# Kernel optimization log

Hardware: AMD Instinct MI355X
Metric: run time of the kernel (lower is better)

The kernel has to match this reference:

```python
import jax, jax.numpy as jnp
import numpy as np


def _bce_with_logits(x, t):
    # numerically-stable binary_cross_entropy_with_logits, reduction='none'
    return jnp.maximum(x, 0.0) - x * t + jnp.log1p(jnp.exp(-jnp.abs(x)))


def _compute_weights(targets):
    """Replicates the scipy.ndimage.label / sum_labels weighting.

    4-connected component labeling (scipy default structure) via iterative
    min-label propagation, then per-pixel component area, then
    1 / (sqrt(area) + 1) with zeros replaced by the global mean of the
    nonzero sqrt-areas.
    """
    B, H, W = targets.shape
    HW = H * W  # sentinel label for background
    fg = targets > 0
    base = jnp.arange(HW, dtype=jnp.int32).reshape(1, H, W)
    lab0 = jnp.where(fg, base, HW).astype(jnp.int32)

    def cond(state):
        return state[1]

    def body(state):
        lab, _ = state
        p = jnp.pad(lab, ((0, 0), (1, 1), (1, 1)), constant_values=HW)
        nb = jnp.minimum(jnp.minimum(p[:, :-2, 1:-1], p[:, 2:, 1:-1]),
                         jnp.minimum(p[:, 1:-1, :-2], p[:, 1:-1, 2:]))
        new = jnp.where(fg, jnp.minimum(lab, nb), HW)
        return new, jnp.any(new != lab)

    lab, _ = jax.lax.while_loop(cond, body, (lab0, jnp.array(True)))

    def per_sample_area(lab_i, fg_i):
        sizes = jax.ops.segment_sum(fg_i.ravel().astype(jnp.float32),
                                    lab_i.ravel(), num_segments=HW + 1)
        return sizes[lab_i]  # [H, W] area of each pixel's component

    area = jax.vmap(per_sample_area)(lab, fg)
    area = jnp.where(fg, area, 0.0)

    w = jnp.sqrt(area)
    nz = w > 0
    # global (whole-tensor) mean of nonzero sqrt-areas, as in the torch code
    mean_nz = jnp.sum(jnp.where(nz, w, 0.0)) / jnp.maximum(
        jnp.sum(nz.astype(jnp.float32)), 1.0)
    w_filled = jnp.where(nz, w, mean_nz)
    return 1.0 / (w_filled + 1.0)


def setup_inputs() -> dict:
    key = jax.random.key(0)
    k1, k2 = jax.random.split(key)
    B, H, W = 32, 512, 512
    inputs = jax.random.normal(k1, (B, H, W), dtype=jnp.float32)
    # sparse binary mask (subcritical density -> small blobs, like vessels)
    targets = (jax.random.uniform(k2, (B, H, W)) < 0.3).astype(jnp.float32)
    return {"inputs": inputs, "targets": targets}


def reference(inputs, targets):
    weights = _compute_weights(targets)
    bce = _bce_with_logits(inputs, targets)
    return jnp.mean(weights * bce)
```

## Files before the change

kernel.cpp:

```cpp
#include <hip/hip_runtime.h>
#include <math.h>

static constexpr int IMG_W  = 512;
static constexpr int IMG_PX = 512 * 512;
static constexpr int NIMG   = 32;
static constexpr int TILE_W = 64;
static constexpr int TILE_H = 32;
static constexpr int TPX    = IMG_W / TILE_W;
static constexpr int TPY    = IMG_W / TILE_H;
static constexpr int TILES_PER_IMG = TPX * TPY;
static constexpr int FUSED_BLOCKS  = NIMG * TILES_PER_IMG;
static constexpr int ECAP_T  = 48;
static constexpr int SCAP    = 128;
static constexpr int NE      = TILES_PER_IMG * ECAP_T;
static constexpr int FLAGBIT = 1 << 30;
static constexpr int CNTMASK = FLAGBIT - 1;
static constexpr int TPIX    = TILE_W * TILE_H;


__device__ __forceinline__ int find_root_l(volatile int* sl, int x) {
    int p = sl[x];
    while (p != x) { x = p; p = sl[x]; }
    return p;
}

__device__ __forceinline__ void merge_l(int* sl, int a, int b) {
    while (true) {
        a = find_root_l(sl, a);
        b = find_root_l(sl, b);
        if (a == b) return;
        if (a < b) { int t = a; a = b; b = t; }
        int old = atomicMin(&sl[a], b);
        if (old == a) return;
        a = old;
    }
}

__device__ __forceinline__ void block_reduce_write(float s_fg, float s_bg,
                                                   float s_sq, float s_n,
                                                   double4* __restrict__ part,
                                                   int slot) {
    for (int o = 32; o > 0; o >>= 1) {
        s_fg += __shfl_down(s_fg, o, 64);
        s_bg += __shfl_down(s_bg, o, 64);
        s_sq += __shfl_down(s_sq, o, 64);
        s_n  += __shfl_down(s_n,  o, 64);
    }
    __shared__ double4 wsum[4];
    int wave = threadIdx.x >> 6;
    if ((threadIdx.x & 63) == 0)
        wsum[wave] = make_double4((double)s_fg, (double)s_bg, (double)s_sq, (double)s_n);
    __syncthreads();
    if (threadIdx.x == 0) {
        double4 b = wsum[0];
        for (int wv = 1; wv < 4; wv++) {
            b.x += wsum[wv].x; b.y += wsum[wv].y;
            b.z += wsum[wv].z; b.w += wsum[wv].w;
        }
        part[slot] = b;
    }
}

__device__ __forceinline__ float bce0_fast(float xx) {
    return fmaxf(xx, 0.f) + __logf(1.f + __expf(-fabsf(xx)));
}


__global__ __launch_bounds__(256) void ccl_fused(const float* __restrict__ t,
                                                 const float* __restrict__ x,
                                                 int* __restrict__ L,
                                                 int2* __restrict__ ilist,
                                                 int* __restrict__ blockcount,
                                                 int2* __restrict__ seams,
                                                 int* __restrict__ seamcount,
                                                 double4* __restrict__ part,
                                                 int* __restrict__ done) {
    __shared__ int   sl[TPIX];
    __shared__ int   cnt[TPIX];
    __shared__ float fsum[TPIX];
    __shared__ unsigned long long rowmask[TILE_H];
    __shared__ int   lcount, scount;

    int blk = blockIdx.x;
    int b   = blk / TILES_PER_IMG;
    int tid = blk % TILES_PER_IMG;
    int tY  = tid / TPX, tX = tid % TPX;
    int k   = threadIdx.x;
    int col = k & 63, wv = k >> 6;
    int base = b * IMG_PX + (tY * TILE_H) * IMG_W + tX * TILE_W;

    if (k == 0) { lcount = 0; scount = 0; }
    if (blk == 0 && k == 0) *done = 0;

    float xr[8];
    unsigned int fgbits = 0;
#pragma unroll
    for (int s = 0; s < 8; s++) {
        int row = wv * 8 + s;
        int jj  = row * TILE_W + col;
        int g   = base + row * IMG_W + col;
        float tv = t[g];
        xr[s] = x[g];
        bool fg = (tv != 0.f);
        fgbits |= (unsigned)fg << s;
        unsigned long long mask = __ballot(fg);
        if (col == 0) rowmask[row] = mask;
        int lab = jj;
        if (fg) {
            unsigned long long startm = mask & ~(mask << 1);
            unsigned long long low = (col == 63) ? ~0ULL : ((1ULL << (col + 1)) - 1ULL);
            lab = row * TILE_W + (63 - __clzll(startm & low));
        }
        sl[jj]   = lab;
        cnt[jj]  = 0;
        fsum[jj] = 0.f;
    }
    __syncthreads();

#pragma unroll
    for (int s = 0; s < 8; s++) {
        int row = wv * 8 + s;
        if (row == 0) continue;
        unsigned long long both = rowmask[row] & rowmask[row - 1];
        unsigned long long pairstart = both & ~(both << 1);
        if ((pairstart >> col) & 1ULL)
            merge_l(sl, row * TILE_W + col, (row - 1) * TILE_W + col);
    }
    __syncthreads();

#pragma unroll
    for (int s = 0; s < 8; s++) {
        int row = wv * 8 + s;
        unsigned long long mask = rowmask[row];
        unsigned long long startm = mask & ~(mask << 1);
        if ((startm >> col) & 1ULL) {
            unsigned long long inv = ~(mask >> col);
            int len = inv ? (__ffsll((long long)inv) - 1) : (64 - col);
            int jj = row * TILE_W + col;
            int r = find_root_l(sl, jj);
            sl[jj] = r;
            atomicAdd(&cnt[r], len);
        }
    }
    __syncthreads();

    {
        int r = -1, c = 0, dg = 0; bool owner = false;
        if      (k < 64)  { r = 0;          c = k;        dg = (tY > 0)       ? -IMG_W : 0; }
        else if (k < 128) { r = TILE_H - 1; c = k - 64;   dg = (tY < TPY - 1) ?  IMG_W : 0; owner = true; }
        else if (k < 160) { r = k - 128;    c = 0;        dg = (tX > 0)       ? -1     : 0; }
        else if (k < 192) { r = k - 160;    c = TILE_W-1; dg = (tX < TPX - 1) ?  1     : 0; owner = true; }
        if (r >= 0) {
            int g = base + r * IMG_W + c;
            bool fg = (rowmask[r] >> c) & 1ULL;
            if (fg) {
                int jj = r * TILE_W + c;
                int root = sl[sl[jj]];
                L[g] = base + (root >> 6) * IMG_W + (root & 63);
                if (dg != 0 && t[g + dg] != 0.f) {
                    atomicOr(&cnt[root], FLAGBIT);
                    if (owner) {
                        int s = atomicAdd(&scount, 1);
                        if (s < SCAP) seams[blk * SCAP + s] = make_int2(g, g + dg);
                    }
                }
            }
        }
    }
    __syncthreads();

    float s_fg = 0.f, s_bg = 0.f, s_sq = 0.f, s_n = 0.f;
#pragma unroll
    for (int s = 0; s < 8; s++) {
        int row = wv * 8 + s;
        int jj  = row * TILE_W + col;
        float xx = xr[s];
        float b0 = bce0_fast(xx);
        int s0   = sl[jj];
        int root = sl[s0];
        int cc   = cnt[root];
        bool fg  = (fgbits >> s) & 1u;
        float bce1 = b0 - xx;
        if (cc & FLAGBIT) {
            atomicAdd(&fsum[root], bce1);
        } else {
            float w   = sqrtf((float)cc);
            float inv = 1.f / (w + 1.f);
            s_fg += fg ? bce1 * inv : 0.f;
            s_bg += fg ? 0.f : b0;
            s_sq += w;
            s_n  += fg ? 1.f : 0.f;
        }
    }
    __syncthreads();

#pragma unroll
    for (int s = 0; s < 8; s++) {
        int jj = (wv * 8 + s) * TILE_W + col;
        if (sl[jj] == jj && (cnt[jj] & FLAGBIT)) {
            int slot = atomicAdd(&lcount, 1);
            if (slot < ECAP_T) {
                ilist[blk * ECAP_T + slot] =
                    make_int2(__float_as_int(fsum[jj]), cnt[jj] & CNTMASK);
                int g = base + (jj >> 6) * IMG_W + (jj & 63);
                L[g] = -(tid * ECAP_T + slot) - 2;
            }
        }
    }
    block_reduce_write(s_fg, s_bg, s_sq, s_n, part, blk);
    if (k == 0) { blockcount[blk] = min(lcount, ECAP_T); seamcount[blk] = min(scount, SCAP); }
}

__global__ __launch_bounds__(1024) void tail(const int* __restrict__ L,
                                             const int2* __restrict__ ilist,
                                             const int* __restrict__ blockcount,
                                             const int2* __restrict__ seams,
                                             const int* __restrict__ seamcount,
                                             const double4* __restrict__ part,
                                             double4* __restrict__ imgpart,
                                             int* __restrict__ done,
                                             float* __restrict__ out,
                                             int N) {
    __shared__ int parent[NE];
    __shared__ int areaL[NE];
    __shared__ int scEx[TILES_PER_IMG + 1];
    __shared__ int bcEx[TILES_PER_IMG + 1];
    int b = blockIdx.x, k = threadIdx.x;
    int tbase = b * TILES_PER_IMG;

    for (int i = k; i < NE; i += 1024) { parent[i] = i; areaL[i] = 0; }
    if (k < TILES_PER_IMG) {
        scEx[k + 1] = seamcount[tbase + k];
        bcEx[k + 1] = blockcount[tbase + k];
    }
    if (k == 0) { scEx[0] = 0; bcEx[0] = 0; }
    __syncthreads();
    for (int off = 1; off < TILES_PER_IMG; off <<= 1) {
        int vs = 0, vb = 0;
        if (k < TILES_PER_IMG && (int)k >= off) {
            vs = scEx[k + 1 - off];
            vb = bcEx[k + 1 - off];
        }
        __syncthreads();
        if (k < TILES_PER_IMG && (int)k >= off) {
            scEx[k + 1] += vs;
            bcEx[k + 1] += vb;
        }
        __syncthreads();
    }
    int nS = scEx[TILES_PER_IMG];
    int nE = bcEx[TILES_PER_IMG];

    for (int i = k; i < nS; i += 1024) {
        int lo = 0, hi = TILES_PER_IMG;
        while (hi - lo > 1) { int mid = (lo + hi) >> 1; if (i >= scEx[mid]) lo = mid; else hi = mid; }
        int slot = i - scEx[lo];
        int2 p = seams[(tbase + lo) * SCAP + slot];
        int v1 = L[p.x]; if (v1 >= 0) v1 = L[v1];
        int v2 = L[p.y]; if (v2 >= 0) v2 = L[v2];
        int e1 = -v1 - 2, e2 = -v2 - 2;
        if (e1 >= 0 && e1 < NE && e2 >= 0 && e2 < NE)
            merge_l(parent, e1, e2);
    }
    __syncthreads();

    for (int i = k; i < nE; i += 1024) {
        int lo = 0, hi = TILES_PER_IMG;
        while (hi - lo > 1) { int mid = (lo + hi) >> 1; if (i >= bcEx[mid]) lo = mid; else hi = mid; }
        int slot = i - bcEx[lo];
        int idx = lo * ECAP_T + slot;
        int2 ent = ilist[(tbase + lo) * ECAP_T + slot];
        atomicAdd(&areaL[find_root_l(parent, idx)], ent.y);
    }
    __syncthreads();

    float s_fg = 0.f, s_sq = 0.f, s_n = 0.f;
    for (int i = k; i < nE; i += 1024) {
        int lo = 0, hi = TILES_PER_IMG;
        while (hi - lo > 1) { int mid = (lo + hi) >> 1; if (i >= bcEx[mid]) lo = mid; else hi = mid; }
        int slot = i - bcEx[lo];
        int idx = lo * ECAP_T + slot;
        int2 ent = ilist[(tbase + lo) * ECAP_T + slot];
        float w = sqrtf((float)areaL[find_root_l(parent, idx)]);
        float c = (float)ent.y;
        s_fg += __int_as_float(ent.x) / (w + 1.f);
        s_sq += c * w;
        s_n  += c;
    }

    double fg = (double)s_fg, bg = 0.0, sq = (double)s_sq, nn = (double)s_n;
    if (k < TILES_PER_IMG) {
        double4 p = part[tbase + k];
        fg += p.x; bg += p.y; sq += p.z; nn += p.w;
    }
    for (int o = 32; o > 0; o >>= 1) {
        fg += __shfl_down(fg, o, 64);
        bg += __shfl_down(bg, o, 64);
        sq += __shfl_down(sq, o, 64);
        nn += __shfl_down(nn, o, 64);
    }
    __shared__ double4 f2[16];
    int wave = k >> 6;
    if ((k & 63) == 0) f2[wave] = make_double4(fg, bg, sq, nn);
    __syncthreads();
    if (k == 0) {
        double4 bb = f2[0];
        for (int wv = 1; wv < 16; wv++) {
            bb.x += f2[wv].x; bb.y += f2[wv].y;
            bb.z += f2[wv].z; bb.w += f2[wv].w;
        }
        imgpart[b] = bb;
    }

    __shared__ int amlast;
    __syncthreads();
    __threadfence();
    if (k == 0) amlast = (atomicAdd(done, 1) == NIMG - 1);
    __syncthreads();
    if (!amlast) return;
    __threadfence();
    double tfg = 0.0, tbg = 0.0, tsq = 0.0, tnn = 0.0;
    if (k < NIMG) {
        double4 p = imgpart[k];
        tfg = p.x; tbg = p.y; tsq = p.z; tnn = p.w;
    }
    if (k < 64) {
        for (int o = 32; o > 0; o >>= 1) {
            tfg += __shfl_down(tfg, o, 64);
            tbg += __shfl_down(tbg, o, 64);
            tsq += __shfl_down(tsq, o, 64);
            tnn += __shfl_down(tnn, o, 64);
        }
        if (k == 0) {
            double mean_nz = tsq / fmax(tnn, 1.0);
            double loss = (tfg + tbg / (mean_nz + 1.0)) / (double)N;
            out[0] = (float)loss;
        }
    }
}


extern "C" void kernel_launch(void* const* d_in, const int* in_sizes, int n_in,
                              void* d_out, int out_size, void* d_ws, size_t ws_size,
                              hipStream_t stream) {
    const float* x = (const float*)d_in[0];
    const float* t = (const float*)d_in[1];
    float* out = (float*)d_out;
    int N = in_sizes[0];

    int* L          = (int*)d_ws;
    double4* part   = (double4*)(L + N);
    double4* imgpart = part + FUSED_BLOCKS;
    int* blockcount = (int*)(imgpart + NIMG);
    int* seamcount  = blockcount + FUSED_BLOCKS;
    int* done       = seamcount + FUSED_BLOCKS;
    int2* ilist     = (int2*)(done + 4);
    int2* seams     = ilist + FUSED_BLOCKS * ECAP_T;

    ccl_fused<<<FUSED_BLOCKS, 256, 0, stream>>>(t, x, L, ilist, blockcount,
                                                seams, seamcount, part, done);
    tail<<<NIMG, 1024, 0, stream>>>(L, ilist, blockcount, seams, seamcount,
                                    part, imgpart, done, out, N);
}
```

Measured before the change: 154.8 us.

## Fuse per-image tail into CCL kernel via last-tile-block election

```diff
diff --git a/kernel.cpp b/kernel.cpp
--- a/kernel.cpp
+++ b/kernel.cpp
@@ -38,6 +38,7 @@
 
 __device__ __forceinline__ void block_reduce_write(float s_fg, float s_bg,
                                                    float s_sq, float s_n,
+                                                   double4* wsum,
                                                    double4* __restrict__ part,
                                                    int slot) {
     for (int o = 32; o > 0; o >>= 1) {
@@ -46,7 +47,6 @@
         s_sq += __shfl_down(s_sq, o, 64);
         s_n  += __shfl_down(s_n,  o, 64);
     }
-    __shared__ double4 wsum[4];
     int wave = threadIdx.x >> 6;
     if ((threadIdx.x & 63) == 0)
         wsum[wave] = make_double4((double)s_fg, (double)s_bg, (double)s_sq, (double)s_n);
@@ -74,12 +74,24 @@
                                                  int2* __restrict__ seams,
                                                  int* __restrict__ seamcount,
                                                  double4* __restrict__ part,
-                                                 int* __restrict__ done) {
-    __shared__ int   sl[TPIX];
-    __shared__ int   cnt[TPIX];
-    __shared__ float fsum[TPIX];
+                                                 double4* __restrict__ imgpart,
+                                                 int* __restrict__ done,
+                                                 float* __restrict__ out,
+                                                 int N) {
+    union SU {
+        struct { int sl[TPIX]; int cnt[TPIX]; float fsum[TPIX]; } c;
+        int parent[NE];
+    };
+    __shared__ SU su;
     __shared__ unsigned long long rowmask[TILE_H];
-    __shared__ int   lcount, scount;
+    __shared__ int   lcount, scount, elect;
+    __shared__ double4 wsum[4];
+    __shared__ int scEx[TILES_PER_IMG + 1];
+    __shared__ int bcEx[TILES_PER_IMG + 1];
+
+    int* sl    = su.c.sl;
+    int* cnt   = su.c.cnt;
+    float* fsum = su.c.fsum;
 
     int blk = blockIdx.x;
     int b   = blk / TILES_PER_IMG;
@@ -90,7 +102,6 @@
     int base = b * IMG_PX + (tY * TILE_H) * IMG_W + tX * TILE_W;
 
     if (k == 0) { lcount = 0; scount = 0; }
-    if (blk == 0 && k == 0) *done = 0;
 
     float xr[8];
     unsigned int fgbits = 0;
@@ -207,28 +218,20 @@
             }
         }
     }
-    block_reduce_write(s_fg, s_bg, s_sq, s_n, part, blk);
+    block_reduce_write(s_fg, s_bg, s_sq, s_n, wsum, part, blk);
     if (k == 0) { blockcount[blk] = min(lcount, ECAP_T); seamcount[blk] = min(scount, SCAP); }
-}
-
-__global__ __launch_bounds__(1024) void tail(const int* __restrict__ L,
-                                             const int2* __restrict__ ilist,
-                                             const int* __restrict__ blockcount,
-                                             const int2* __restrict__ seams,
-                                             const int* __restrict__ seamcount,
-                                             const double4* __restrict__ part,
-                                             double4* __restrict__ imgpart,
-                                             int* __restrict__ done,
-                                             float* __restrict__ out,
-                                             int N) {
-    __shared__ int parent[NE];
-    __shared__ int areaL[NE];
-    __shared__ int scEx[TILES_PER_IMG + 1];
-    __shared__ int bcEx[TILES_PER_IMG + 1];
-    int b = blockIdx.x, k = threadIdx.x;
+
+    __syncthreads();
+    __threadfence();
+    if (k == 0) elect = (atomicAdd(&done[b], 1) == TILES_PER_IMG - 1);
+    __syncthreads();
+    if (!elect) return;
+    __threadfence();
+
+    int* parent = su.parent;
     int tbase = b * TILES_PER_IMG;
 
-    for (int i = k; i < NE; i += 1024) { parent[i] = i; areaL[i] = 0; }
+    for (int i = k; i < NE; i += 256) parent[i] = i;
     if (k < TILES_PER_IMG) {
         scEx[k + 1] = seamcount[tbase + k];
         bcEx[k + 1] = blockcount[tbase + k];
@@ -237,12 +240,12 @@
     __syncthreads();
     for (int off = 1; off < TILES_PER_IMG; off <<= 1) {
         int vs = 0, vb = 0;
-        if (k < TILES_PER_IMG && (int)k >= off) {
+        if (k < TILES_PER_IMG && k >= off) {
             vs = scEx[k + 1 - off];
             vb = bcEx[k + 1 - off];
         }
         __syncthreads();
-        if (k < TILES_PER_IMG && (int)k >= off) {
+        if (k < TILES_PER_IMG && k >= off) {
             scEx[k + 1] += vs;
             bcEx[k + 1] += vb;
         }
@@ -251,11 +254,11 @@
     int nS = scEx[TILES_PER_IMG];
     int nE = bcEx[TILES_PER_IMG];
 
-    for (int i = k; i < nS; i += 1024) {
+    for (int i = k; i < nS; i += 256) {
         int lo = 0, hi = TILES_PER_IMG;
         while (hi - lo > 1) { int mid = (lo + hi) >> 1; if (i >= scEx[mid]) lo = mid; else hi = mid; }
         int slot = i - scEx[lo];
-        int2 p = seams[(tbase + lo) * SCAP + slot];
+        int2 p = seams[(size_t)(tbase + lo) * SCAP + slot];
         int v1 = L[p.x]; if (v1 >= 0) v1 = L[v1];
         int v2 = L[p.y]; if (v2 >= 0) v2 = L[v2];
         int e1 = -v1 - 2, e2 = -v2 - 2;
@@ -264,31 +267,35 @@
     }
     __syncthreads();
 
-    for (int i = k; i < nE; i += 1024) {
+    int* areaG = (int*)(seams + (size_t)tbase * SCAP);
+    for (int i = k; i < NE; i += 256) areaG[i] = 0;
+    __syncthreads();
+
+    for (int i = k; i < nE; i += 256) {
         int lo = 0, hi = TILES_PER_IMG;
         while (hi - lo > 1) { int mid = (lo + hi) >> 1; if (i >= bcEx[mid]) lo = mid; else hi = mid; }
         int slot = i - bcEx[lo];
         int idx = lo * ECAP_T + slot;
-        int2 ent = ilist[(tbase + lo) * ECAP_T + slot];
-        atomicAdd(&areaL[find_root_l(parent, idx)], ent.y);
-    }
-    __syncthreads();
-
-    float s_fg = 0.f, s_sq = 0.f, s_n = 0.f;
-    for (int i = k; i < nE; i += 1024) {
+        int2 ent = ilist[(size_t)(tbase + lo) * ECAP_T + slot];
+        atomicAdd(&areaG[find_root_l(parent, idx)], ent.y);
+    }
+    __syncthreads();
+
+    float t_fg = 0.f, t_sq = 0.f, t_n = 0.f;
+    for (int i = k; i < nE; i += 256) {
         int lo = 0, hi = TILES_PER_IMG;
         while (hi - lo > 1) { int mid = (lo + hi) >> 1; if (i >= bcEx[mid]) lo = mid; else hi = mid; }
         int slot = i - bcEx[lo];
         int idx = lo * ECAP_T + slot;
-        int2 ent = ilist[(tbase + lo) * ECAP_T + slot];
-        float w = sqrtf((float)areaL[find_root_l(parent, idx)]);
+        int2 ent = ilist[(size_t)(tbase + lo) * ECAP_T + slot];
+        float w = sqrtf((float)areaG[find_root_l(parent, idx)]);
         float c = (float)ent.y;
-        s_fg += __int_as_float(ent.x) / (w + 1.f);
-        s_sq += c * w;
-        s_n  += c;
-    }
-
-    double fg = (double)s_fg, bg = 0.0, sq = (double)s_sq, nn = (double)s_n;
+        t_fg += __int_as_float(ent.x) / (w + 1.f);
+        t_sq += c * w;
+        t_n  += c;
+    }
+
+    double fg = (double)t_fg, bg = 0.0, sq = (double)t_sq, nn = (double)t_n;
     if (k < TILES_PER_IMG) {
         double4 p = part[tbase + k];
         fg += p.x; bg += p.y; sq += p.z; nn += p.w;
@@ -299,26 +306,25 @@
         sq += __shfl_down(sq, o, 64);
         nn += __shfl_down(nn, o, 64);
     }
-    __shared__ double4 f2[16];
     int wave = k >> 6;
-    if ((k & 63) == 0) f2[wave] = make_double4(fg, bg, sq, nn);
+    if ((k & 63) == 0) wsum[wave] = make_double4(fg, bg, sq, nn);
     __syncthreads();
     if (k == 0) {
-        double4 bb = f2[0];
-        for (int wv = 1; wv < 16; wv++) {
-            bb.x += f2[wv].x; bb.y += f2[wv].y;
-            bb.z += f2[wv].z; bb.w += f2[wv].w;
+        double4 bb = wsum[0];
+        for (int wv2 = 1; wv2 < 4; wv2++) {
+            bb.x += wsum[wv2].x; bb.y += wsum[wv2].y;
+            bb.z += wsum[wv2].z; bb.w += wsum[wv2].w;
         }
         imgpart[b] = bb;
     }
 
-    __shared__ int amlast;
     __syncthreads();
     __threadfence();
-    if (k == 0) amlast = (atomicAdd(done, 1) == NIMG - 1);
-    __syncthreads();
-    if (!amlast) return;
+    if (k == 0) elect = (atomicAdd(&done[NIMG], 1) == NIMG - 1);
+    __syncthreads();
+    if (!elect) return;
     __threadfence();
+
     double tfg = 0.0, tbg = 0.0, tsq = 0.0, tnn = 0.0;
     if (k < NIMG) {
         double4 p = imgpart[k];
@@ -354,11 +360,12 @@
     int* blockcount = (int*)(imgpart + NIMG);
     int* seamcount  = blockcount + FUSED_BLOCKS;
     int* done       = seamcount + FUSED_BLOCKS;
-    int2* ilist     = (int2*)(done + 4);
+    int2* ilist     = (int2*)(done + 64);
     int2* seams     = ilist + FUSED_BLOCKS * ECAP_T;
 
+    hipMemsetAsync(done, 0, (NIMG + 1) * sizeof(int), stream);
+
     ccl_fused<<<FUSED_BLOCKS, 256, 0, stream>>>(t, x, L, ilist, blockcount,
-                                                seams, seamcount, part, done);
-    tail<<<NIMG, 1024, 0, stream>>>(L, ilist, blockcount, seams, seamcount,
-                                    part, imgpart, done, out, N);
-}
+                                                seams, seamcount, part,
+                                                imgpart, done, out, N);
+}
```

Result: slower. 551.2 us (+256.2%).
